# Optimization experiments

Measured on AMD Instinct MI355X. Metric: run time of the kernel, lower is better.

The kernel has to match this reference:

```python
import jax, jax.numpy as jnp
import numpy as np

B, N, T, E, EH, C = 32, 500, 13, 2000, 300, 40
EPS = 1e-5


def _bn_noaffine(x):
    m = x.mean(axis=(0, 2, 3), keepdims=True)
    v = x.var(axis=(0, 2, 3), keepdims=True)
    return (x - m) * jax.lax.rsqrt(v + EPS)


def _bn(x, g, b):
    return g[None, :, None, None] * _bn_noaffine(x) + b[None, :, None, None]


def _conv1x1(x, W, b):
    # x: [B,Cin,N,T], W: [Cout,Cin]
    return jnp.einsum('bcnt,oc->bont', x, W) + b[None, :, None, None]


def _dconv(x, W, b, dil=2):
    # dilated causal conv, kernel (1,2): W [Cout,Cin,2]
    y = jnp.einsum('bcnt,oc->bont', x[..., :-dil], W[:, :, 0])
    y = y + jnp.einsum('bcnt,oc->bont', x[..., dil:], W[:, :, 1])
    return y + b[None, :, None, None]


def setup_inputs() -> dict:
    key = jax.random.key(0)
    ks = jax.random.split(key, 24)
    d = {}
    d['input'] = jax.random.normal(ks[0], (B, 1, N, T), jnp.float32)
    d['A_fwd'] = jax.random.uniform(ks[1], (N, N), jnp.float32) / N
    d['A_bwd'] = jax.random.uniform(ks[2], (N, N), jnp.float32) / N
    d['indices'] = jax.random.randint(ks[3], (2, E), 0, N, jnp.int32)
    d['G0_all'] = jax.random.uniform(ks[4], (E, EH), jnp.float32) * 0.01
    d['G1_all'] = jax.random.uniform(ks[5], (EH, E), jnp.float32) * 0.01
    d['nodevec1'] = jax.random.normal(ks[6], (N, 10), jnp.float32)
    d['nodevec2'] = jax.random.normal(ks[7], (10, N), jnp.float32)
    d['w_edge_f'] = jax.random.uniform(ks[8], (EH,), jnp.float32)
    d['w_edge_b'] = jax.random.uniform(ks[9], (EH,), jnp.float32)
    d['vsrc_f'] = jax.random.normal(ks[10], (3, C), jnp.float32) * 0.05
    d['vdst_f'] = jax.random.normal(ks[11], (3, C), jnp.float32) * 0.05
    d['vsrc_b'] = jax.random.normal(ks[12], (3, C), jnp.float32) * 0.05
    d['vdst_b'] = jax.random.normal(ks[13], (3, C), jnp.float32) * 0.05
    d['start_w'] = jax.random.normal(ks[14], (C, 1), jnp.float32)
    d['start_b'] = jnp.zeros((C,), jnp.float32)
    d['filter_w'] = jax.random.normal(ks[15], (3, C, C, 2), jnp.float32) * (1.0 / np.sqrt(2 * C))
    d['filter_b'] = jnp.zeros((3, C), jnp.float32)
    d['gate_w'] = jax.random.normal(ks[16], (3, C, C, 2), jnp.float32) * (1.0 / np.sqrt(2 * C))
    d['gate_b'] = jnp.zeros((3, C), jnp.float32)
    d['gconv_w'] = jax.random.normal(ks[17], (3, 7 * C, C), jnp.float32) * (1.0 / np.sqrt(7 * C))
    d['gconv_b'] = jnp.zeros((3, C), jnp.float32)
    d['bn_g_gamma'] = jnp.ones((3, C), jnp.float32)
    d['bn_g_beta'] = jnp.zeros((3, C), jnp.float32)
    d['bn_gamma'] = jnp.ones((3, C), jnp.float32)
    d['bn_beta'] = jnp.zeros((3, C), jnp.float32)
    d['skip_w'] = jax.random.normal(ks[18], (3, 320, C), jnp.float32) * (1.0 / np.sqrt(C))
    d['skip_b'] = jnp.zeros((3, 320), jnp.float32)
    d['end1_w'] = jax.random.normal(ks[19], (640, 320), jnp.float32) * (1.0 / np.sqrt(320))
    d['end1_b'] = jnp.zeros((640,), jnp.float32)
    d['end2_w'] = jax.random.normal(ks[20], (12, 640), jnp.float32) * (1.0 / np.sqrt(640))
    d['end2_b'] = jnp.zeros((12,), jnp.float32)
    return d


def reference(input, A_fwd, A_bwd, indices, G0_all, G1_all, nodevec1, nodevec2,
              w_edge_f, w_edge_b, vsrc_f, vdst_f, vsrc_b, vdst_b,
              start_w, start_b, filter_w, filter_b, gate_w, gate_b,
              gconv_w, gconv_b, bn_g_gamma, bn_g_beta, bn_gamma, bn_beta,
              skip_w, skip_b, end1_w, end1_b, end2_w, end2_b):
    x = _bn_noaffine(input)
    x = _conv1x1(x, start_w, start_b)
    b, _, n, _ = x.shape
    # adaptive adjacency: softmax(relu(V1 @ V2)) over rows (torch dim=1 on [N,N])
    adp = jax.nn.softmax(jax.nn.relu(nodevec1 @ nodevec2), axis=1)
    # hypergraph edge-to-edge diffusion operators: G0 @ diag(w) @ G1  ->  [E,E]
    GG_f = G0_all @ (w_edge_f[:, None] * G1_all)
    GG_b = G0_all @ (w_edge_b[:, None] * G1_all)
    i0, i1 = indices[0], indices[1]
    eye = jnp.eye(n, dtype=x.dtype)
    skip = None
    for blk in range(3):
        # dynamic edge scores from node features (mean over time)
        xmean = x.mean(axis=3)                              # [B,C,N]
        src = xmean[:, :, i0]                               # [B,C,E]
        dst = xmean[:, :, i1]
        sc_f = jnp.einsum('bce,c->be', src, vsrc_f[blk]) + jnp.einsum('bce,c->be', dst, vdst_f[blk])
        sc_b = jnp.einsum('bce,c->be', src, vsrc_b[blk]) + jnp.einsum('bce,c->be', dst, vdst_b[blk])
        ef = jax.nn.sigmoid(sc_f @ GG_f)                    # [B,E]
        eb = jax.nn.sigmoid(sc_b @ GG_b)
        # identity medium with sigmoid edge weights scattered at the edge indices
        Mf = jnp.broadcast_to(eye, (b, n, n)).at[:, i0, i1].set(ef)
        Mb = jnp.broadcast_to(eye, (b, n, n)).at[:, i0, i1].set(eb)
        s0 = Mf * A_fwd[None]                               # [B,N,N]
        s1 = jnp.swapaxes(Mb, 1, 2) * A_bwd[None]
        s2 = jnp.broadcast_to(adp, (b, n, n))
        residual = x
        f = jnp.tanh(_dconv(residual, filter_w[blk], filter_b[blk]))
        g = jax.nn.sigmoid(_dconv(residual, gate_w[blk], gate_b[blk]))
        x = f * g
        # diffusion graph conv, order 2, over 3 batched supports
        outs = [x]
        for A in (s0, s1, s2):
            x1 = jnp.einsum('bcnt,bnm->bcmt', x, A)
            outs.append(x1)
            outs.append(jnp.einsum('bcnt,bnm->bcmt', x1, A))
        h = jnp.concatenate(outs, axis=1)                   # [B,7C,N,T']
        x = jnp.einsum('bcnt,co->bont', h, gconv_w[blk]) + gconv_b[blk][None, :, None, None]
        x = _bn(x, bn_g_gamma[blk], bn_g_beta[blk])
        x = x + residual[:, :, :, -x.shape[3]:]
        x = _bn(x, bn_gamma[blk], bn_beta[blk])
        s = _conv1x1(x, skip_w[blk], skip_b[blk])
        skip = s if skip is None else s + skip[:, :, :, -s.shape[3]:]
    x = jax.nn.leaky_relu(skip)
    x = jax.nn.leaky_relu(_conv1x1(x, end1_w, end1_b))
    x = _conv1x1(x, end2_w, end2_b)
    return x
```

## Files before the change

### kernel.cpp

```cpp
#include <hip/hip_runtime.h>
#include <hip/hip_bf16.h>

constexpr int B_  = 32;
constexpr int N_  = 500;
constexpr int T0_ = 13;
constexpr int E_  = 2000;
constexpr int EH_ = 300;
constexpr int C_  = 40;
constexpr float EPS_ = 1e-5f;
constexpr int KP_ = 512;

typedef short bf16x8 __attribute__((ext_vector_type(8)));
typedef _Float16 f16x8 __attribute__((ext_vector_type(8)));
typedef _Float16 f16x4 __attribute__((ext_vector_type(4)));
typedef float f32x4  __attribute__((ext_vector_type(4)));

__device__ __forceinline__ float sigm(float x){ return 1.f/(1.f+__expf(-x)); }
__device__ __forceinline__ float lrelu(float x){ return x > 0.f ? x : 0.01f*x; }
__device__ __forceinline__ unsigned short f2bf(float f){
    __hip_bfloat16 h = __float2bfloat16(f);
    return *(unsigned short*)&h;
}
__device__ __forceinline__ float bf2f(unsigned short us){
    __hip_bfloat16 h = *(__hip_bfloat16*)&us;
    return __bfloat162float(h);
}

__global__ __launch_bounds__(256) void kern_init(float* __restrict__ insum, int* __restrict__ map,
                                                 int* __restrict__ cnts, int* __restrict__ selfe,
                                                 int* __restrict__ adpTbz)
{
    int i = blockIdx.x*256 + threadIdx.x;
    if (i < 2) insum[i] = 0.f;
    if (i < N_*N_) map[i] = -1;
    if (i < 1024) cnts[i] = 0;
    if (i < 512) selfe[i] = -1;
    if (i < KP_*KP_/2) adpTbz[i] = 0;
}

__global__ __launch_bounds__(256) void kern_zeroacc(float* __restrict__ p, int n)
{
    int i = blockIdx.x*256 + threadIdx.x;
    if (i < n) p[i] = 0.f;
}

__global__ __launch_bounds__(256) void kern_instats(const float* __restrict__ in, float* __restrict__ acc)
{
    float s = 0.f, ss = 0.f;
    int total = B_*N_*T0_;
    for (int i = blockIdx.x*256 + threadIdx.x; i < total; i += gridDim.x*256) {
        float v = in[i]; s += v; ss += v*v;
    }
    __shared__ float l1[256], l2[256];
    l1[threadIdx.x] = s; l2[threadIdx.x] = ss; __syncthreads();
    for (int o = 128; o > 0; o >>= 1) {
        if (threadIdx.x < o) { l1[threadIdx.x] += l1[threadIdx.x+o]; l2[threadIdx.x] += l2[threadIdx.x+o]; }
        __syncthreads();
    }
    if (threadIdx.x == 0) { atomicAdd(&acc[0], l1[0]); atomicAdd(&acc[1], l2[0]); }
}

__global__ __launch_bounds__(256) void kern_x0(const float* __restrict__ in, const float* __restrict__ insum,
    const float* __restrict__ sw, const float* __restrict__ sb, float* __restrict__ x)
{
    int idx = blockIdx.x*256 + threadIdx.x;
    int total = B_*N_*T0_*C_;
    if (idx >= total) return;
    float cnt = (float)(B_*N_*T0_);
    float mean = insum[0]/cnt;
    float var  = insum[1]/cnt - mean*mean;
    float inv  = rsqrtf(var + EPS_);
    int c = idx % C_;
    int pos = idx / C_;
    float xn = (in[pos] - mean)*inv;
    x[idx] = sw[c]*xn + sb[c];
}

__global__ __launch_bounds__(512) void kern_adp(const float* __restrict__ nv1, const float* __restrict__ nv2,
                                                __hip_bfloat16* __restrict__ adpTb)
{
    int n = blockIdx.x;
    int m = threadIdx.x;
    float r = 0.f;
    if (m < N_) {
        #pragma unroll
        for (int k = 0; k < 10; ++k) r += nv1[n*10+k]*nv2[k*N_+m];
        r = r > 0.f ? r : 0.f;
    }
    __shared__ float red[512];
    red[threadIdx.x] = (m < N_) ? r : -1e30f; __syncthreads();
    for (int o = 256; o > 0; o >>= 1) {
        if (threadIdx.x < o) red[threadIdx.x] = fmaxf(red[threadIdx.x], red[threadIdx.x+o]);
        __syncthreads();
    }
    float mx = red[0]; __syncthreads();
    float ev = (m < N_) ? __expf(r - mx) : 0.f;
    red[threadIdx.x] = ev; __syncthreads();
    for (int o = 256; o > 0; o >>= 1) {
        if (threadIdx.x < o) red[threadIdx.x] += red[threadIdx.x+o];
        __syncthreads();
    }
    float sum = red[0];
    if (m < N_) adpTb[(size_t)m*KP_ + n] = __float2bfloat16(ev/sum);
}

__global__ void kern_emax(const int* __restrict__ idx, int* __restrict__ map)
{
    int e = blockIdx.x*256 + threadIdx.x;
    if (e < E_) atomicMax(&map[idx[e]*N_ + idx[E_+e]], e);
}
__global__ void kern_ecnt(const int* __restrict__ idx, const int* __restrict__ map,
                          int* __restrict__ cnt0, int* __restrict__ cnt1, int* __restrict__ selfe)
{
    int e = blockIdx.x*256 + threadIdx.x;
    if (e >= E_) return;
    int i0 = idx[e], i1 = idx[E_+e];
    if (map[i0*N_+i1] != e) return;
    atomicAdd(&cnt1[i1], 1);
    atomicAdd(&cnt0[i0], 1);
    if (i0 == i1) selfe[i0] = e;
}
__global__ __launch_bounds__(512) void kern_scan(const int* __restrict__ cnt0, const int* __restrict__ cnt1,
    int* __restrict__ ptr0, int* __restrict__ ptr1, int* __restrict__ cur0, int* __restrict__ cur1)
{
    __shared__ int s0[512], s1[512];
    int tid = threadIdx.x;
    s0[tid] = (tid < N_) ? cnt0[tid] : 0;
    s1[tid] = (tid < N_) ? cnt1[tid] : 0;
    __syncthreads();
    for (int o = 1; o < 512; o <<= 1) {
        int v0 = (tid >= o) ? s0[tid-o] : 0;
        int v1 = (tid >= o) ? s1[tid-o] : 0;
        __syncthreads();
        s0[tid] += v0; s1[tid] += v1;
        __syncthreads();
    }
    if (tid == 0) { ptr0[0] = 0; ptr1[0] = 0; }
    if (tid < N_) {
        ptr0[tid+1] = s0[tid]; ptr1[tid+1] = s1[tid];
        cur0[tid] = (tid == 0) ? 0 : s0[tid-1];
        cur1[tid] = (tid == 0) ? 0 : s1[tid-1];
    }
}
__global__ void kern_efill(const int* __restrict__ idx, const int* __restrict__ map,
    const float* __restrict__ Af, const float* __restrict__ Ab,
    int* __restrict__ cur0, int* __restrict__ cur1,
    int* __restrict__ e0id, int* __restrict__ e0nb, float* __restrict__ a0v,
    int* __restrict__ e1id, int* __restrict__ e1nb, float* __restrict__ a1v)
{
    int e = blockIdx.x*256 + threadIdx.x;
    if (e >= E_) return;
    int i0 = idx[e], i1 = idx[E_+e];
    if (map[i0*N_+i1] != e) return;
    int s1 = atomicAdd(&cur1[i1], 1);
    e0id[s1] = e; e0nb[s1] = i0; a0v[s1] = Af[i0*N_+i1];
    int s0 = atomicAdd(&cur0[i0], 1);
    e1id[s0] = e; e1nb[s0] = i1; a1v[s0] = Ab[i1*N_+i0];
}

__global__ __launch_bounds__(64) void kern_umean(const float* __restrict__ x, int Tin,
    const float* __restrict__ vsf, const float* __restrict__ vdf,
    const float* __restrict__ vsb, const float* __restrict__ vdb,
    float* __restrict__ usf, float* __restrict__ udf, float* __restrict__ usb, float* __restrict__ udb)
{
    int bn = blockIdx.x;
    const float* xp = x + (size_t)bn*Tin*C_;
    int tid = threadIdx.x;
    float a0=0.f,a1=0.f,a2=0.f,a3=0.f;
    for (int i = tid; i < Tin*C_; i += 64) {
        float v = xp[i]; int c = i % C_;
        a0 += v*vsf[c]; a1 += v*vdf[c]; a2 += v*vsb[c]; a3 += v*vdb[c];
    }
    for (int o = 32; o > 0; o >>= 1) {
        a0 += __shfl_down(a0,o); a1 += __shfl_down(a1,o);
        a2 += __shfl_down(a2,o); a3 += __shfl_down(a3,o);
    }
    if (tid == 0) {
        float inv = 1.f/(float)Tin;
        usf[bn]=a0*inv; udf[bn]=a1*inv; usb[bn]=a2*inv; udb[bn]=a3*inv;
    }
}

__global__ __launch_bounds__(320) void kern_t(const int* __restrict__ idx,
    const float* __restrict__ usf, const float* __restrict__ udf,
    const float* __restrict__ usb, const float* __restrict__ udb,
    const float* __restrict__ G0, float* __restrict__ tf, float* __restrict__ tb,
    float* __restrict__ scf, float* __restrict__ scb)
{
    int b = blockIdx.x, chunk = blockIdx.y;
    int e0 = chunk*250;
    __shared__ float sf[250], sb2[250];
    int tid = threadIdx.x;
    for (int i = tid; i < 250; i += 320) {
        int e = e0 + i;
        int i0 = idx[e], i1 = idx[E_+e];
        float vf = usf[b*N_+i0] + udf[b*N_+i1];
        float vb = usb[b*N_+i0] + udb[b*N_+i1];
        sf[i] = vf; sb2[i] = vb;
        scf[b*E_+e] = vf; scb[b*E_+e] = vb;
    }
    __syncthreads();
    if (tid < EH_) {
        float af = 0.f, ab = 0.f;
        for (int i = 0; i < 250; ++i) {
            float g = G0[(size_t)(e0+i)*EH_ + tid];
            af += sf[i]*g; ab += sb2[i]*g;
        }
        atomicAdd(&tf[b*EH_+tid], af);
        atomicAdd(&tb[b*EH_+tid], ab);
    }
}

__global__ __launch_bounds__(256) void kern_ef(const float* __restrict__ tf, const float* __restrict__ tb,
    const float* __restrict__ wf, const float* __restrict__ wb, const float* __restrict__ G1,
    float* __restrict__ ef, float* __restrict__ eb)
{
    int b = blockIdx.y;
    int e = blockIdx.x*256 + threadIdx.x;
    __shared__ float f[EH_], g[EH_];
    for (int i = threadIdx.x; i < EH_; i += 256) {
        f[i] = tf[b*EH_+i]*wf[i];
        g[i] = tb[b*EH_+i]*wb[i];
    }
    __syncthreads();
    if (e < E_) {
        float af = 0.f, ab = 0.f;
        for (int h = 0; h < EH_; ++h) {
            float v = G1[(size_t)h*E_ + e];
            af += f[h]*v; ab += g[h]*v;
        }
        ef[b*E_+e] = sigm(af);
        eb[b*E_+e] = sigm(ab);
    }
}

__global__ __launch_bounds__(256) void kern_dconv_acc(const float* __restrict__ x, int Tin,
    const float* __restrict__ fw, const float* __restrict__ fb4,
    const float* __restrict__ gw, const float* __restrict__ gb4,
    const float* __restrict__ wl0, const float* __restrict__ gbias,
    float* __restrict__ xg, float* __restrict__ gc,
    __hip_bfloat16* __restrict__ xgT, int JP)
{
    int Tout = Tin - 2;
    int nout = Tout*C_;
    int tile = threadIdx.x >> 7;
    int lane = threadIdx.x & 127;
    int bn = blockIdx.x*2 + tile;
    int b = bn / N_, n = bn % N_;
    __shared__ alignas(16) float xs[2][T0_*C_];
    __shared__ alignas(16) float wf[2*C_*C_];
    __shared__ alignas(16) float wg[2*C_*C_];
    __shared__ alignas(16) float wl[C_*C_];
    __shared__ alignas(16) float ps[2][11*C_];
    int tid = threadIdx.x;
    {
        const float4* xp = (const float4*)(x + (size_t)bn*Tin*C_);
        float4* xd = (float4*)xs[tile];
        for (int i = lane; i < (Tin*C_)/4; i += 128) xd[i] = xp[i];
    }
    for (int i = tid; i < 2*C_*C_; i += 256) {
        int k = i / (C_*C_); int r = i % (C_*C_); int c = r / C_; int o = r % C_;
        wf[i] = fw[(o*C_+c)*2 + k];
        wg[i] = gw[(o*C_+c)*2 + k];
    }
    for (int i = tid; i < C_*C_; i += 256) wl[i] = wl0[i];
    __syncthreads();
    int nq = Tout*10;
    for (int u = lane; u < nq; u += 128) {
        int t = u/10, o = (u%10)*4;
        float4 f4 = *(const float4*)&fb4[o];
        float4 g4 = *(const float4*)&gb4[o];
        for (int c = 0; c < C_; ++c) {
            float x0v = xs[tile][t*C_+c], x2v = xs[tile][(t+2)*C_+c];
            float4 wf0 = *(const float4*)&wf[c*C_+o];
            float4 wf1 = *(const float4*)&wf[C_*C_ + c*C_+o];
            float4 wg0 = *(const float4*)&wg[c*C_+o];
            float4 wg1 = *(const float4*)&wg[C_*C_ + c*C_+o];
            f4.x += wf0.x*x0v + wf1.x*x2v;  f4.y += wf0.y*x0v + wf1.y*x2v;
            f4.z += wf0.z*x0v + wf1.z*x2v;  f4.w += wf0.w*x0v + wf1.w*x2v;
            g4.x += wg0.x*x0v + wg1.x*x2v;  g4.y += wg0.y*x0v + wg1.y*x2v;
            g4.z += wg0.z*x0v + wg1.z*x2v;  g4.w += wg0.w*x0v + wg1.w*x2v;
        }
        float4 r4;
        r4.x = tanhf(f4.x)*sigm(g4.x);
        r4.y = tanhf(f4.y)*sigm(g4.y);
        r4.z = tanhf(f4.z)*sigm(g4.z);
        r4.w = tanhf(f4.w)*sigm(g4.w);
        *(float4*)&ps[tile][t*C_+o] = r4;
        *(float4*)&xg[(size_t)bn*nout + t*C_+o] = r4;
        int j = t*C_+o;
        size_t tb = ((size_t)b*JP + j)*KP_ + n;
        xgT[tb]          = __float2bfloat16(r4.x);
        xgT[tb + KP_]    = __float2bfloat16(r4.y);
        xgT[tb + 2*KP_]  = __float2bfloat16(r4.z);
        xgT[tb + 3*KP_]  = __float2bfloat16(r4.w);
    }
    __syncthreads();
    for (int u = lane; u < nq; u += 128) {
        int t = u/10, o = (u%10)*4;
        float4 a4 = *(const float4*)&gbias[o];
        for (int c = 0; c < C_; ++c) {
            float s = ps[tile][t*C_+c];
            float4 w = *(const float4*)&wl[c*C_+o];
            a4.x += s*w.x; a4.y += s*w.y; a4.z += s*w.z; a4.w += s*w.w;
        }
        *(float4*)&gc[(size_t)bn*nout + t*C_+o] = a4;
    }
}

__global__ __launch_bounds__(256) void kern_sparse_acc(const float* __restrict__ in,
    float* __restrict__ outTile, int Tout,
    const int* __restrict__ ptr, const int* __restrict__ nbr, const int* __restrict__ eid,
    const float* __restrict__ aval, const float* __restrict__ coef,
    const float* __restrict__ Amat, const int* __restrict__ selfe,
    const float* __restrict__ gwp, float* __restrict__ gc)
{
    int tile = threadIdx.x >> 7;
    int lane = threadIdx.x & 127;
    int bn = blockIdx.x*2 + tile;
    int b = bn / N_, m = bn % N_;
    __shared__ float wv[2][64];
    __shared__ int   nb[2][64];
    __shared__ alignas(16) float ps[2][11*C_];
    __shared__ alignas(16) float wl[C_*C_];
    int tid = threadIdx.x;
    int p0 = ptr[m], p1 = ptr[m+1];
    int deg = p1 - p0; if (deg > 64) deg = 64;
    if (lane < deg) {
        wv[tile][lane] = coef[b*E_ + eid[p0+lane]] * aval[p0+lane];
        nb[tile][lane] = nbr[p0+lane];
    }
    for (int i = tid; i < C_*C_; i += 256) wl[i] = gwp[i];
    __syncthreads();
    float dval = (selfe[m] >= 0) ? 0.f : Amat[(size_t)m*N_ + m];
    const float* inb = in + (size_t)b*N_*Tout*C_;
    int nout = Tout*C_;
    for (int oi = lane; oi < nout; oi += 128) {
        float acc = dval * inb[(size_t)m*nout + oi];
        for (int j = 0; j < deg; ++j) acc += wv[tile][j]*inb[(size_t)nb[tile][j]*nout + oi];
        ps[tile][oi] = acc;
        if (outTile) outTile[(size_t)bn*nout + oi] = acc;
    }
    __syncthreads();
    int nq = Tout*10;
    for (int u = lane; u < nq; u += 128) {
        int t = u/10, o = (u%10)*4;
        float4 a4 = *(const float4*)&gc[(size_t)bn*nout + t*C_+o];
        for (int c = 0; c < C_; ++c) {
            float s = ps[tile][t*C_+c];
            float4 w = *(const float4*)&wl[c*C_+o];
            a4.x += s*w.x; a4.y += s*w.y; a4.z += s*w.z; a4.w += s*w.w;
        }
        *(float4*)&gc[(size_t)bn*nout + t*C_+o] = a4;
    }
}

__global__ __launch_bounds__(256) void kern_gemm_mfma(const __hip_bfloat16* __restrict__ adpTb,
    const __hip_bfloat16* __restrict__ inT, float* __restrict__ outF,
    __hip_bfloat16* __restrict__ outT, int LD, int JP)
{
    int tid = threadIdx.x;
    int wave = tid >> 6, lane = tid & 63;
    int rn = lane & 15, q = lane >> 4;
    int b = blockIdx.z;
    int m0 = blockIdx.x*64;
    int j0 = blockIdx.y*64;
    const short* Ap = (const short*)adpTb + (size_t)(m0 + wave*16 + rn)*KP_ + q*8;
    bf16x8 areg[16];
    #pragma unroll
    for (int kk = 0; kk < 16; ++kk) areg[kk] = *(const bf16x8*)(Ap + kk*32);
    const short* Bp = (const short*)inT + ((size_t)b*JP + j0 + rn)*KP_ + q*8;
    f32x4 acc[4] = {};
    #pragma unroll
    for (int kk = 0; kk < 16; ++kk) {
        #pragma unroll
        for (int s = 0; s < 4; ++s) {
            bf16x8 bb = *(const bf16x8*)(Bp + (size_t)s*16*KP_ + kk*32);
            acc[s] = __builtin_amdgcn_mfma_f32_16x16x32_bf16(areg[kk], bb, acc[s], 0, 0, 0);
        }
    }
    int mb = m0 + wave*16 + q*4;
    #pragma unroll
    for (int s = 0; s < 4; ++s) {
        int j = j0 + s*16 + rn;
        if (j >= LD) continue;
        #pragma unroll
        for (int r = 0; r < 4; ++r) {
            int m = mb + r;
            if (m < N_) outF[((size_t)b*N_ + m)*LD + j] = acc[s][r];
        }
        if (outT) {
            ushort4 v;
            v.x = f2bf(acc[s][0]); v.y = f2bf(acc[s][1]);
            v.z = f2bf(acc[s][2]); v.w = f2bf(acc[s][3]);
            *(ushort4*)((unsigned short*)outT + ((size_t)b*JP + j)*KP_ + mb) = v;
        }
    }
}

__global__ __launch_bounds__(256) void kern_gacc(const float* __restrict__ part, const float* __restrict__ gwp,
    float* __restrict__ gc, int Tout)
{
    int tile = threadIdx.x >> 7;
    int lane = threadIdx.x & 127;
    int bn = blockIdx.x*2 + tile;
    int nout = Tout*C_;
    __shared__ alignas(16) float ps[2][11*C_];
    __shared__ alignas(16) float wl[C_*C_];
    int tid = threadIdx.x;
    {
        const float4* pp = (const float4*)(part + (size_t)bn*nout);
        float4* pd = (float4*)ps[tile];
        for (int i = lane; i < nout/4; i += 128) pd[i] = pp[i];
    }
    for (int i = tid; i < C_*C_; i += 256) wl[i] = gwp[i];
    __syncthreads();
    int nq = Tout*10;
    for (int u = lane; u < nq; u += 128) {
        int t = u/10, o = (u%10)*4;
        float4 a4 = *(const float4*)&gc[(size_t)bn*nout + t*C_+o];
        for (int c = 0; c < C_; ++c) {
            float s = ps[tile][t*C_+c];
            float4 w = *(const float4*)&wl[c*C_+o];
            a4.x += s*w.x; a4.y += s*w.y; a4.z += s*w.z; a4.w += s*w.w;
        }
        *(float4*)&gc[(size_t)bn*nout + t*C_+o] = a4;
    }
}

__global__ __launch_bounds__(320) void kern_bnstats(const float* __restrict__ src, size_t total, float* __restrict__ acc)
{
    int tid = threadIdx.x;
    float s = 0.f, ss = 0.f;
    for (size_t i = (size_t)blockIdx.x*320 + tid; i < total; i += (size_t)gridDim.x*320) {
        float v = src[i]; s += v; ss += v*v;
    }
    __shared__ float ls[320], lss[320];
    ls[tid] = s; lss[tid] = ss; __syncthreads();
    if (tid < C_) {
        float t1 = 0.f, t2 = 0.f;
        for (int r = 0; r < 8; ++r) { t1 += ls[r*C_+tid]; t2 += lss[r*C_+tid]; }
        atomicAdd(&acc[tid], t1); atomicAdd(&acc[C_+tid], t2);
    }
}

__global__ __launch_bounds__(320) void kern_bn1(float* __restrict__ gc, const float* __restrict__ resid,
    int Tin, int Tout, const float* __restrict__ acc1,
    const float* __restrict__ g1, const float* __restrict__ b1, float* __restrict__ acc2)
{
    int tid = threadIdx.x; int c = tid % C_;
    float cnt = (float)(B_*N_*Tout);
    float mean = acc1[c]/cnt;
    float var  = acc1[C_+c]/cnt - mean*mean;
    float inv  = rsqrtf(var + EPS_);
    float gg = g1[c], bb = b1[c];
    int dlt = Tin - Tout;
    float s = 0.f, ss = 0.f;
    size_t total = (size_t)B_*N_*Tout*C_;
    for (size_t i = (size_t)blockIdx.x*320 + tid; i < total; i += (size_t)gridDim.x*320) {
        size_t pos = i / C_; int t = (int)(pos % Tout); size_t bn = pos / Tout;
        float y = gg*(gc[i]-mean)*inv + bb;
        y += resid[(bn*Tin + (t+dlt))*C_ + c];
        gc[i] = y;
        s += y; ss += y*y;
    }
    __shared__ float ls[320], lss[320];
    ls[tid] = s; lss[tid] = ss; __syncthreads();
    if (tid < C_) {
        float t1 = 0.f, t2 = 0.f;
        for (int r = 0; r < 8; ++r) { t1 += ls[r*C_+tid]; t2 += lss[r*C_+tid]; }
        atomicAdd(&acc2[tid], t1); atomicAdd(&acc2[C_+tid], t2);
    }
}

__global__ __launch_bounds__(256) void kern_bn2(const float* __restrict__ gc, float* __restrict__ xout, int Tout,
    const float* __restrict__ acc2, const float* __restrict__ g2, const float* __restrict__ b2)
{
    size_t total = (size_t)B_*N_*Tout*C_;
    size_t i = (size_t)blockIdx.x*256 + threadIdx.x;
    if (i >= total) return;
    int c = (int)(i % C_);
    float cnt = (float)(B_*N_*Tout);
    float mean = acc2[c]/cnt;
    float var  = acc2[C_+c]/cnt - mean*mean;
    float inv  = rsqrtf(var + EPS_);
    xout[i] = g2[c]*(gc[i]-mean)*inv + b2[c];
}

__global__ __launch_bounds__(256) void kern_skip(const float* __restrict__ x, int Tout,
    const float* __restrict__ sw, const float* __restrict__ sbias, __hip_bfloat16* __restrict__ skp, int first,
    const float* __restrict__ acc2, const float* __restrict__ g2, const float* __restrict__ b2)
{
    int bn0 = blockIdx.x*4; int half = blockIdx.y;
    int off = Tout - 7;
    __shared__ alignas(16) float xs[4][7*C_];
    __shared__ alignas(16) float wl[C_*164];
    __shared__ float scl[C_], bia[C_];
    int tid = threadIdx.x;
    if (acc2) {
        if (tid < C_) {
            float cnt = (float)(B_*N_*Tout);
            float mean = acc2[tid]/cnt;
            float var  = acc2[C_+tid]/cnt - mean*mean;
            float inv  = rsqrtf(var + EPS_);
            scl[tid] = g2[tid]*inv;
            bia[tid] = b2[tid] - g2[tid]*mean*inv;
        }
        __syncthreads();
    }
    for (int i = tid; i < 4*(7*C_/4); i += 256) {
        int bl = i / 70, r = i % 70;
        float4 v = ((const float4*)(x + ((size_t)(bn0+bl)*Tout + off)*C_))[r];
        if (acc2) {
            int c0 = (r*4) % C_;
            v.x = scl[c0]*v.x + bia[c0];
            v.y = scl[c0+1]*v.y + bia[c0+1];
            v.z = scl[c0+2]*v.z + bia[c0+2];
            v.w = scl[c0+3]*v.w + bia[c0+3];
        }
        ((float4*)xs[bl])[r] = v;
    }
    for (int i = tid; i < 160*C_; i += 256) {
        int oo = i / C_, c = i % C_;
        wl[c*164 + oo] = sw[(size_t)(half*160 + oo)*C_ + c];
    }
    __syncthreads();
    for (int u = tid; u < 4*7*40; u += 256) {
        int bl = u / 280; int v = u % 280;
        int t = v / 40, o = (v % 40)*4;
        float4 a4 = {0.f,0.f,0.f,0.f};
        for (int c = 0; c < C_; ++c) {
            float s = xs[bl][t*C_+c];
            float4 w = *(const float4*)&wl[c*164 + o];
            a4.x += s*w.x; a4.y += s*w.y; a4.z += s*w.z; a4.w += s*w.w;
        }
        int og = half*160 + o;
        float4 b4 = *(const float4*)&sbias[og];
        a4.x += b4.x; a4.y += b4.y; a4.z += b4.z; a4.w += b4.w;
        size_t di = ((size_t)(bn0+bl)*7 + t)*320 + og;
        if (first) {
            skp[di+0] = __float2bfloat16(a4.x);
            skp[di+1] = __float2bfloat16(a4.y);
            skp[di+2] = __float2bfloat16(a4.z);
            skp[di+3] = __float2bfloat16(a4.w);
        } else {
            skp[di+0] = __float2bfloat16(__bfloat162float(skp[di+0]) + a4.x);
            skp[di+1] = __float2bfloat16(__bfloat162float(skp[di+1]) + a4.y);
            skp[di+2] = __float2bfloat16(__bfloat162float(skp[di+2]) + a4.z);
            skp[di+3] = __float2bfloat16(__bfloat162float(skp[di+3]) + a4.w);
        }
    }
}

__global__ __launch_bounds__(256) void kern_cvtw(const float* __restrict__ w, __hip_bfloat16* __restrict__ wb, int n)
{
    int i = blockIdx.x*256 + threadIdx.x;
    if (i < n) wb[i] = __float2bfloat16(w[i]);
}

constexpr int ASD_ = 324;
__global__ __launch_bounds__(256, 2) void kern_end2(const __hip_bfloat16* __restrict__ skp,
    const __hip_bfloat16* __restrict__ e1wb, const float* __restrict__ e1b,
    const float* __restrict__ e2w, const float* __restrict__ e2b, float* __restrict__ out)
{
    __shared__ short As[64*ASD_];
    __shared__ _Float16 w2h[640][12];
    int tid = threadIdx.x;
    int wave = tid >> 6, lane = tid & 63;
    int rn = lane & 15, q = lane >> 4;
    int m0 = blockIdx.x*64;
    {
        const bf16x8* gA = (const bf16x8*)((const short*)skp + (size_t)m0*320);
        for (int i = tid; i < 2560; i += 256) {
            bf16x8 v = gA[i];
            bf16x8 r;
            #pragma unroll
            for (int e = 0; e < 8; ++e)
                r[e] = (short)f2bf(lrelu(bf2f((unsigned short)v[e])));
            int row = i / 40, col = (i % 40)*8;
            *(bf16x8*)&As[row*ASD_ + col] = r;
        }
    }
    for (int i = tid; i < 640*12; i += 256) {
        int c = i / 12, o = i % 12;
        w2h[c][o] = (_Float16)e2w[o*640 + c];
    }
    __syncthreads();
    const short* Arow = As + (wave*16 + rn)*ASD_ + q*8;
    float acc_out[4][12] = {};
    const short* e1p = (const short*)e1wb;
    #pragma unroll 1
    for (int csp = 0; csp < 20; ++csp) {
        const short* Bp0 = e1p + (size_t)(csp*32 + rn)*320 + q*8;
        const short* Bp1 = Bp0 + 16*320;
        f32x4 c00 = {}, c01 = {}, c10 = {}, c11 = {};
        #pragma unroll
        for (int kk = 0; kk < 10; kk += 2) {
            bf16x8 a0 = *(const bf16x8*)(Arow + kk*32);
            bf16x8 a1 = *(const bf16x8*)(Arow + (kk+1)*32);
            bf16x8 b00 = *(const bf16x8*)(Bp0 + kk*32);
            bf16x8 b01 = *(const bf16x8*)(Bp0 + (kk+1)*32);
            bf16x8 b10 = *(const bf16x8*)(Bp1 + kk*32);
            bf16x8 b11 = *(const bf16x8*)(Bp1 + (kk+1)*32);
            c00 = __builtin_amdgcn_mfma_f32_16x16x32_bf16(a0, b00, c00, 0, 0, 0);
            c10 = __builtin_amdgcn_mfma_f32_16x16x32_bf16(a0, b10, c10, 0, 0, 0);
            c01 = __builtin_amdgcn_mfma_f32_16x16x32_bf16(a1, b01, c01, 0, 0, 0);
            c11 = __builtin_amdgcn_mfma_f32_16x16x32_bf16(a1, b11, c11, 0, 0, 0);
        }
        int ca = csp*32 + rn, cb = ca + 16;
        float bias0 = e1b[ca], bias1 = e1b[cb];
        f16x4 wa0 = *(const f16x4*)&w2h[ca][0];
        f16x4 wa1 = *(const f16x4*)&w2h[ca][4];
        f16x4 wa2 = *(const f16x4*)&w2h[ca][8];
        f16x4 wb0 = *(const f16x4*)&w2h[cb][0];
        f16x4 wb1 = *(const f16x4*)&w2h[cb][4];
        f16x4 wb2 = *(const f16x4*)&w2h[cb][8];
        #pragma unroll
        for (int r = 0; r < 4; ++r) {
            float y0 = lrelu(c00[r] + c01[r] + bias0);
            float y1 = lrelu(c10[r] + c11[r] + bias1);
            #pragma unroll
            for (int o = 0; o < 4; ++o) {
                acc_out[r][o]   += y0*(float)wa0[o] + y1*(float)wb0[o];
                acc_out[r][4+o] += y0*(float)wa1[o] + y1*(float)wb1[o];
                acc_out[r][8+o] += y0*(float)wa2[o] + y1*(float)wb2[o];
            }
        }
    }
    #pragma unroll
    for (int r = 0; r < 4; ++r)
        #pragma unroll
        for (int o = 0; o < 12; ++o) {
            float v = acc_out[r][o];
            v += __shfl_xor(v, 1);
            v += __shfl_xor(v, 2);
            v += __shfl_xor(v, 4);
            v += __shfl_xor(v, 8);
            acc_out[r][o] = v;
        }
    if (rn < 12) {
        float bo = e2b[rn];
        #pragma unroll
        for (int r = 0; r < 4; ++r) {
            float v = 0.f;
            #pragma unroll
            for (int o = 0; o < 12; ++o) v = (rn == o) ? acc_out[r][o] : v;
            int gm = m0 + wave*16 + q*4 + r;
            int t = gm % 7; int bn = gm / 7; int n = bn % N_; int b = bn / N_;
            out[(((size_t)b*12 + rn)*N_ + n)*7 + t] = v + bo;
        }
    }
}

extern "C" void kernel_launch(void* const* d_in, const int* in_sizes, int n_in,
                              void* d_out, int out_size, void* d_ws, size_t ws_size,
                              hipStream_t stream)
{
    (void)in_sizes; (void)n_in; (void)out_size;
    const float* input   = (const float*)d_in[0];
    const float* A_fwd   = (const float*)d_in[1];
    const float* A_bwd   = (const float*)d_in[2];
    const int*   indices = (const int*)  d_in[3];
    const float* G0      = (const float*)d_in[4];
    const float* G1      = (const float*)d_in[5];
    const float* nv1     = (const float*)d_in[6];
    const float* nv2     = (const float*)d_in[7];
    const float* wef     = (const float*)d_in[8];
    const float* web     = (const float*)d_in[9];
    const float* vsf     = (const float*)d_in[10];
    const float* vdf     = (const float*)d_in[11];
    const float* vsb     = (const float*)d_in[12];
    const float* vdb     = (const float*)d_in[13];
    const float* start_w = (const float*)d_in[14];
    const float* start_b = (const float*)d_in[15];
    const float* filt_w  = (const float*)d_in[16];
    const float* filt_b  = (const float*)d_in[17];
    const float* gate_w  = (const float*)d_in[18];
    const float* gate_b  = (const float*)d_in[19];
    const float* gcw     = (const float*)d_in[20];
    const float* gcb     = (const float*)d_in[21];
    const float* bng_g   = (const float*)d_in[22];
    const float* bng_b   = (const float*)d_in[23];
    const float* bn_g    = (const float*)d_in[24];
    const float* bn_b    = (const float*)d_in[25];
    const float* skw     = (const float*)d_in[26];
    const float* skb     = (const float*)d_in[27];
    const float* e1w     = (const float*)d_in[28];
    const float* e1b     = (const float*)d_in[29];
    const float* e2w     = (const float*)d_in[30];
    const float* e2b     = (const float*)d_in[31];
    float* out = (float*)d_out;

    float* W = (float*)d_ws;
    size_t off = 0;
    auto FA = [&](size_t n){ off = (off + 3) & ~(size_t)3; float* p = W + off; off += n; return p; };
    float* insum  = FA(2);
    float* tf     = FA((size_t)B_*EH_);
    float* tb     = FA((size_t)B_*EH_);
    float* bnacc1 = FA(80);
    float* bnacc2 = FA(80);
    float* usf = FA((size_t)B_*N_); float* udf = FA((size_t)B_*N_);
    float* usb = FA((size_t)B_*N_); float* udb = FA((size_t)B_*N_);
    float* scf = FA((size_t)B_*E_); float* scb = FA((size_t)B_*E_);
    float* efv = FA((size_t)B_*E_); float* ebv = FA((size_t)B_*E_);
    __hip_bfloat16* adpTb = (__hip_bfloat16*)FA((size_t)KP_*KP_/2);
    float* a0v = FA(E_); float* a1v = FA(E_);
    int* map  = (int*)FA((size_t)N_*N_);
    int* cnt0 = (int*)FA(512); int* cnt1 = (int*)FA(512);
    int* ptr0 = (int*)FA(512); int* ptr1 = (int*)FA(512);
    int* cur0 = (int*)FA(512); int* cur1 = (int*)FA(512);
    int* selfe = (int*)FA(512);
    int* e0id = (int*)FA(E_); int* e0nb = (int*)FA(E_);
    int* e1id = (int*)FA(E_); int* e1nb = (int*)FA(E_);
    float* xA  = FA((size_t)B_*N_*T0_*C_);
    float* xg  = FA((size_t)B_*N_*11*C_);
    float* pa  = FA((size_t)B_*N_*11*C_);
    float* gc  = FA((size_t)B_*N_*11*C_);
    __hip_bfloat16* skp = (__hip_bfloat16*)FA((size_t)B_*N_*7*320/2);
    __hip_bfloat16* xgT = (__hip_bfloat16*)FA((size_t)B_*448*KP_/2);
    __hip_bfloat16* paT = (__hip_bfloat16*)FA((size_t)B_*448*KP_/2);
    __hip_bfloat16* e1wb = (__hip_bfloat16*)xg;

    if (ws_size < off*sizeof(float)) return;

    kern_init<<<(N_*N_+255)/256, 256, 0, stream>>>(insum, map, cnt0, selfe, (int*)adpTb);
    kern_instats<<<256, 256, 0, stream>>>(input, insum);
    kern_x0<<<(B_*N_*T0_*C_+255)/256, 256, 0, stream>>>(input, insum, start_w, start_b, xA);
    kern_adp<<<N_, 512, 0, stream>>>(nv1, nv2, adpTb);
    kern_emax<<<(E_+255)/256, 256, 0, stream>>>(indices, map);
    kern_ecnt<<<(E_+255)/256, 256, 0, stream>>>(indices, map, cnt0, cnt1, selfe);
    kern_scan<<<1, 512, 0, stream>>>(cnt0, cnt1, ptr0, ptr1, cur0, cur1);
    kern_efill<<<(E_+255)/256, 256, 0, stream>>>(indices, map, A_fwd, A_bwd, cur0, cur1,
                                                 e0id, e0nb, a0v, e1id, e1nb, a1v);

    for (int blk = 0; blk < 3; ++blk) {
        int Tin = T0_ - 2*blk;
        int Tout = Tin - 2;
        int LD = Tout*C_;
        int JP = (LD + 63) & ~63;
        size_t total = (size_t)B_*N_*Tout*C_;
        kern_zeroacc<<<(2*B_*EH_+160+255)/256, 256, 0, stream>>>(tf, 2*B_*EH_+160);

        kern_umean<<<B_*N_, 64, 0, stream>>>(xA, Tin, vsf+blk*C_, vdf+blk*C_, vsb+blk*C_, vdb+blk*C_,
                                             usf, udf, usb, udb);
        kern_t<<<dim3(B_, 8), 320, 0, stream>>>(indices, usf, udf, usb, udb, G0, tf, tb, scf, scb);
        kern_ef<<<dim3(8, B_), 256, 0, stream>>>(tf, tb, wef, web, G1, efv, ebv);

        const float* gwb = gcw + (size_t)blk*7*C_*C_;
        kern_dconv_acc<<<B_*N_/2, 256, 0, stream>>>(xA, Tin,
            filt_w + (size_t)blk*2*C_*C_, filt_b + blk*C_,
            gate_w + (size_t)blk*2*C_*C_, gate_b + blk*C_,
            gwb + 0*C_*C_, gcb + blk*C_, xg, gc, xgT, JP);
        kern_sparse_acc<<<B_*N_/2, 256, 0, stream>>>(xg, pa, Tout, ptr1, e0nb, e0id, a0v, efv,
                                                     A_fwd, selfe, gwb + 1*C_*C_, gc);
        kern_sparse_acc<<<B_*N_/2, 256, 0, stream>>>(pa, nullptr, Tout, ptr1, e0nb, e0id, a0v, efv,
                                                     A_fwd, selfe, gwb + 2*C_*C_, gc);
        kern_sparse_acc<<<B_*N_/2, 256, 0, stream>>>(xg, pa, Tout, ptr0, e1nb, e1id, a1v, ebv,
                                                     A_bwd, selfe, gwb + 3*C_*C_, gc);
        kern_sparse_acc<<<B_*N_/2, 256, 0, stream>>>(pa, nullptr, Tout, ptr0, e1nb, e1id, a1v, ebv,
                                                     A_bwd, selfe, gwb + 4*C_*C_, gc);
        dim3 gg(8, JP/64, B_);
        kern_gemm_mfma<<<gg, 256, 0, stream>>>(adpTb, xgT, pa, paT, LD, JP);
        kern_gacc<<<B_*N_/2, 256, 0, stream>>>(pa, gwb + 5*C_*C_, gc, Tout);
        kern_gemm_mfma<<<gg, 256, 0, stream>>>(adpTb, paT, xg, nullptr, LD, JP);
        kern_gacc<<<B_*N_/2, 256, 0, stream>>>(xg, gwb + 6*C_*C_, gc, Tout);

        kern_bnstats<<<512, 320, 0, stream>>>(gc, total, bnacc1);
        kern_bn1<<<512, 320, 0, stream>>>(gc, xA, Tin, Tout, bnacc1, bng_g + blk*C_, bng_b + blk*C_, bnacc2);
        if (blk < 2) {
            kern_bn2<<<(int)((total+255)/256), 256, 0, stream>>>(gc, xA, Tout, bnacc2, bn_g + blk*C_, bn_b + blk*C_);
            kern_skip<<<dim3(B_*N_/4, 2), 256, 0, stream>>>(xA, Tout, skw + (size_t)blk*320*C_, skb + blk*320,
                                                            skp, blk == 0 ? 1 : 0, nullptr, nullptr, nullptr);
        } else {
            kern_skip<<<dim3(B_*N_/4, 2), 256, 0, stream>>>(gc, Tout, skw + (size_t)blk*320*C_, skb + blk*320,
                                                            skp, 0, bnacc2, bn_g + blk*C_, bn_b + blk*C_);
        }
    }

    kern_cvtw<<<(640*320+255)/256, 256, 0, stream>>>(e1w, e1wb, 640*320);
    kern_end2<<<B_*N_*7/64, 256, 0, stream>>>(skp, e1wb, e1b, e2w, e2b, out);
}
```

Measured before the change: 2.532 ms.

## Split end head across hidden-channel blocks with atomic accumulation into output

The fused end1/end2 kernel now parallelizes over the 640 hidden channels as well as rows. Each block handles 64 hidden channels for 64 rows, keeps the activated skip rows in registers instead of LDS, and atomically adds its partial end2 contribution into an output pre-filled with bias by a new init kernel. This raises the block count tenfold and removes the large LDS tile. In exchange it recomputes the leaky-relu on the A rows in every channel block, adds float atomics and an extra launch, and makes the summation order nondeterministic.

```diff
diff --git a/kernel.cpp b/kernel.cpp
--- a/kernel.cpp
+++ b/kernel.cpp
@@ -558,72 +558,64 @@
     if (i < n) wb[i] = __float2bfloat16(w[i]);
 }
 
-constexpr int ASD_ = 324;
-__global__ __launch_bounds__(256, 2) void kern_end2(const __hip_bfloat16* __restrict__ skp,
+__global__ void kern_oinit(float* __restrict__ out, const float* __restrict__ e2b)
+{
+    int i = blockIdx.x*256 + threadIdx.x;
+    if (i >= B_*12*N_*7) return;
+    int o = (i / (N_*7)) % 12;
+    out[i] = e2b[o];
+}
+
+__global__ __launch_bounds__(256) void kern_endf(const __hip_bfloat16* __restrict__ skp,
     const __hip_bfloat16* __restrict__ e1wb, const float* __restrict__ e1b,
-    const float* __restrict__ e2w, const float* __restrict__ e2b, float* __restrict__ out)
-{
-    __shared__ short As[64*ASD_];
-    __shared__ _Float16 w2h[640][12];
+    const float* __restrict__ e2w, float* __restrict__ out)
+{
+    __shared__ _Float16 w2h[64][12];
     int tid = threadIdx.x;
     int wave = tid >> 6, lane = tid & 63;
     int rn = lane & 15, q = lane >> 4;
-    int m0 = blockIdx.x*64;
-    {
-        const bf16x8* gA = (const bf16x8*)((const short*)skp + (size_t)m0*320);
-        for (int i = tid; i < 2560; i += 256) {
-            bf16x8 v = gA[i];
-            bf16x8 r;
-            #pragma unroll
-            for (int e = 0; e < 8; ++e)
-                r[e] = (short)f2bf(lrelu(bf2f((unsigned short)v[e])));
-            int row = i / 40, col = (i % 40)*8;
-            *(bf16x8*)&As[row*ASD_ + col] = r;
-        }
-    }
-    for (int i = tid; i < 640*12; i += 256) {
-        int c = i / 12, o = i % 12;
-        w2h[c][o] = (_Float16)e2w[o*640 + c];
-    }
-    __syncthreads();
-    const short* Arow = As + (wave*16 + rn)*ASD_ + q*8;
+    int c0 = blockIdx.x*64;
+    int m0 = blockIdx.y*64;
+    for (int i = tid; i < 64*12; i += 256) {
+        int cc = i / 12, o = i % 12;
+        w2h[cc][o] = (_Float16)e2w[o*640 + c0 + cc];
+    }
+    __syncthreads();
+    const short* Ap = (const short*)skp + (size_t)(m0 + wave*16 + rn)*320 + q*8;
+    bf16x8 areg[10];
+    #pragma unroll
+    for (int kk = 0; kk < 10; ++kk) {
+        bf16x8 v = *(const bf16x8*)(Ap + kk*32);
+        bf16x8 r;
+        #pragma unroll
+        for (int e = 0; e < 8; ++e) r[e] = (short)f2bf(lrelu(bf2f((unsigned short)v[e])));
+        areg[kk] = r;
+    }
+    const short* Bp = (const short*)e1wb + (size_t)(c0 + rn)*320 + q*8;
+    f32x4 acc[4] = {};
+    #pragma unroll
+    for (int kk = 0; kk < 10; ++kk) {
+        #pragma unroll
+        for (int s = 0; s < 4; ++s) {
+            bf16x8 bb = *(const bf16x8*)(Bp + (size_t)s*16*320 + kk*32);
+            acc[s] = __builtin_amdgcn_mfma_f32_16x16x32_bf16(areg[kk], bb, acc[s], 0, 0, 0);
+        }
+    }
     float acc_out[4][12] = {};
-    const short* e1p = (const short*)e1wb;
-    #pragma unroll 1
-    for (int csp = 0; csp < 20; ++csp) {
-        const short* Bp0 = e1p + (size_t)(csp*32 + rn)*320 + q*8;
-        const short* Bp1 = Bp0 + 16*320;
-        f32x4 c00 = {}, c01 = {}, c10 = {}, c11 = {};
-        #pragma unroll
-        for (int kk = 0; kk < 10; kk += 2) {
-            bf16x8 a0 = *(const bf16x8*)(Arow + kk*32);
-            bf16x8 a1 = *(const bf16x8*)(Arow + (kk+1)*32);
-            bf16x8 b00 = *(const bf16x8*)(Bp0 + kk*32);
-            bf16x8 b01 = *(const bf16x8*)(Bp0 + (kk+1)*32);
-            bf16x8 b10 = *(const bf16x8*)(Bp1 + kk*32);
-            bf16x8 b11 = *(const bf16x8*)(Bp1 + (kk+1)*32);
-            c00 = __builtin_amdgcn_mfma_f32_16x16x32_bf16(a0, b00, c00, 0, 0, 0);
-            c10 = __builtin_amdgcn_mfma_f32_16x16x32_bf16(a0, b10, c10, 0, 0, 0);
-            c01 = __builtin_amdgcn_mfma_f32_16x16x32_bf16(a1, b01, c01, 0, 0, 0);
-            c11 = __builtin_amdgcn_mfma_f32_16x16x32_bf16(a1, b11, c11, 0, 0, 0);
-        }
-        int ca = csp*32 + rn, cb = ca + 16;
-        float bias0 = e1b[ca], bias1 = e1b[cb];
-        f16x4 wa0 = *(const f16x4*)&w2h[ca][0];
-        f16x4 wa1 = *(const f16x4*)&w2h[ca][4];
-        f16x4 wa2 = *(const f16x4*)&w2h[ca][8];
-        f16x4 wb0 = *(const f16x4*)&w2h[cb][0];
-        f16x4 wb1 = *(const f16x4*)&w2h[cb][4];
-        f16x4 wb2 = *(const f16x4*)&w2h[cb][8];
+    #pragma unroll
+    for (int s = 0; s < 4; ++s) {
+        float bias = e1b[c0 + s*16 + rn];
+        f16x4 w0 = *(const f16x4*)&w2h[s*16+rn][0];
+        f16x4 w1 = *(const f16x4*)&w2h[s*16+rn][4];
+        f16x4 w2v = *(const f16x4*)&w2h[s*16+rn][8];
         #pragma unroll
         for (int r = 0; r < 4; ++r) {
-            float y0 = lrelu(c00[r] + c01[r] + bias0);
-            float y1 = lrelu(c10[r] + c11[r] + bias1);
+            float y = lrelu(acc[s][r] + bias);
             #pragma unroll
             for (int o = 0; o < 4; ++o) {
-                acc_out[r][o]   += y0*(float)wa0[o] + y1*(float)wb0[o];
-                acc_out[r][4+o] += y0*(float)wa1[o] + y1*(float)wb1[o];
-                acc_out[r][8+o] += y0*(float)wa2[o] + y1*(float)wb2[o];
+                acc_out[r][o]   += y*(float)w0[o];
+                acc_out[r][4+o] += y*(float)w1[o];
+                acc_out[r][8+o] += y*(float)w2v[o];
             }
         }
     }
@@ -639,7 +631,6 @@
             acc_out[r][o] = v;
         }
     if (rn < 12) {
-        float bo = e2b[rn];
         #pragma unroll
         for (int r = 0; r < 4; ++r) {
             float v = 0.f;
@@ -647,7 +638,7 @@
             for (int o = 0; o < 12; ++o) v = (rn == o) ? acc_out[r][o] : v;
             int gm = m0 + wave*16 + q*4 + r;
             int t = gm % 7; int bn = gm / 7; int n = bn % N_; int b = bn / N_;
-            out[(((size_t)b*12 + rn)*N_ + n)*7 + t] = v + bo;
+            atomicAdd(&out[(((size_t)b*12 + rn)*N_ + n)*7 + t], v);
         }
     }
 }
@@ -778,5 +769,6 @@
     }
 
     kern_cvtw<<<(640*320+255)/256, 256, 0, stream>>>(e1w, e1wb, 640*320);
-    kern_end2<<<B_*N_*7/64, 256, 0, stream>>>(skp, e1wb, e1b, e2w, e2b, out);
-}
+    kern_oinit<<<(B_*12*N_*7+255)/256, 256, 0, stream>>>(out, e2b);
+    kern_endf<<<dim3(10, B_*N_*7/64), 256, 0, stream>>>(skp, e1wb, e1b, e2w, out);
+}
```

New measurement: 2.653 ms. 1.05x slower.
